# Performance work log

Measured on AMD Instinct MI355X. Metric: run time of the kernel, lower is better.

## Reference

```python
import jax, jax.numpy as jnp
import numpy as np
import math
from jax import lax

L, E, H, F = 4, 1024, 16, 4096
B, S = 8, 512
VV, VR = 40, 30
DIST_V = 200
PAD_ID = 0


def setup_inputs() -> dict:
    key = jax.random.key(0)
    ks = iter(jax.random.split(key, 32))
    w = lambda *sh: jax.random.normal(next(ks), sh, jnp.float32) * 0.02
    inp = {
        'val_emb': w(VV, E),
        'ring_emb': w(VR, E),
        'dist_emb': w(DIST_V, H),
        'Wqkv': w(L, 3 * E, E), 'bqkv': jnp.zeros((L, 3 * E), jnp.float32),
        'Wo': w(L, E, E), 'bo': jnp.zeros((L, E), jnp.float32),
        'ln1_s': jnp.ones((L, E), jnp.float32), 'ln1_b': jnp.zeros((L, E), jnp.float32),
        'W1': w(L, F, E), 'b1': jnp.zeros((L, F), jnp.float32),
        'W2': w(L, E, F), 'b2': jnp.zeros((L, E), jnp.float32),
        'ln2_s': jnp.ones((L, E), jnp.float32), 'ln2_b': jnp.zeros((L, E), jnp.float32),
        'lnf_s': jnp.ones((E,), jnp.float32), 'lnf_b': jnp.zeros((E,), jnp.float32),
        'gen_W': w(VV * VR, E), 'gen_b': jnp.zeros((VV * VR,), jnp.float32),
    }
    val = jax.random.randint(next(ks), (B, S), 0, VV)
    val = val.at[:, 0].set(1)  # ensure first key is never <pad> (id 0)
    inp['val_sequences'] = val
    inp['ring_sequences'] = jax.random.randint(next(ks), (B, S), 0, VR)
    inp['distance_squares'] = jax.random.randint(next(ks), (B, S, S), 0, DIST_V)
    return inp


def _ln(x, s, b):
    m = x.mean(-1, keepdims=True)
    v = ((x - m) ** 2).mean(-1, keepdims=True)
    return (x - m) / jnp.sqrt(v + 1e-5) * s + b


def _forward(val_emb, ring_emb, dist_emb, Wqkv, bqkv, Wo, bo, ln1_s, ln1_b,
             W1, b1, W2, b2, ln2_s, ln2_b, lnf_s, lnf_b, gen_W, gen_b,
             val_sequences, ring_sequences, distance_squares):
    Bv, Sv = val_sequences.shape
    dh = E // H
    scale = 1.0 / math.sqrt(dh)
    # token embeddings, each scaled by sqrt(emb_size)
    x = (val_emb[val_sequences] + ring_emb[ring_sequences]) * math.sqrt(E)  # [B,S,E]
    # distance bias [B,S,S,H] -> [B,H,S,S], causal fill with -inf, key padding -inf
    bias = jnp.transpose(dist_emb[distance_squares], (0, 3, 1, 2))
    causal = jnp.tril(jnp.ones((Sv, Sv), bool))
    mask = jnp.where(causal[None, None], bias, -jnp.inf)
    pad = (val_sequences == PAD_ID)  # [B,S]
    mask = jnp.where(pad[:, None, None, :], -jnp.inf, mask)

    def step(h, p):
        wqkv, bq, wo, bo_, l1s, l1b, w1, b1_, w2, b2_, l2s, l2b = p
        qkv = h @ wqkv.T + bq  # [B,S,3E]
        q, k, v = jnp.split(qkv, 3, axis=-1)
        q = q.reshape(Bv, Sv, H, dh).transpose(0, 2, 1, 3)
        k = k.reshape(Bv, Sv, H, dh).transpose(0, 2, 1, 3)
        v = v.reshape(Bv, Sv, H, dh).transpose(0, 2, 1, 3)
        scores = jnp.einsum('bhqd,bhkd->bhqk', q, k) * scale + mask
        a = jax.nn.softmax(scores, axis=-1)
        ctx = jnp.einsum('bhqk,bhkd->bhqd', a, v)
        ctx = ctx.transpose(0, 2, 1, 3).reshape(Bv, Sv, E)
        h = _ln(h + ctx @ wo.T + bo_, l1s, l1b)  # post-norm
        ff = jax.nn.gelu(h @ w1.T + b1_, approximate=False) @ w2.T + b2_
        h = _ln(h + ff, l2s, l2b)
        return h, None

    layer_params = (Wqkv, bqkv, Wo, bo, ln1_s, ln1_b, W1, b1, W2, b2, ln2_s, ln2_b)
    x, _ = lax.scan(step, x, layer_params)
    x = _ln(x, lnf_s, lnf_b)
    return x @ gen_W.T + gen_b  # [B,S,VV*VR]


def reference(val_emb, ring_emb, dist_emb, Wqkv, bqkv, Wo, bo, ln1_s, ln1_b,
              W1, b1, W2, b2, ln2_s, ln2_b, lnf_s, lnf_b, gen_W, gen_b,
              val_sequences, ring_sequences, distance_squares):
    return _forward(val_emb, ring_emb, dist_emb, Wqkv, bqkv, Wo, bo, ln1_s, ln1_b,
                    W1, b1, W2, b2, ln2_s, ln2_b, lnf_s, lnf_b, gen_W, gen_b,
                    val_sequences, ring_sequences, distance_squares)
```

## Files before the change

### kernel.cpp

```cpp
#include <hip/hip_runtime.h>
#include <hip/hip_bf16.h>

typedef __attribute__((ext_vector_type(8))) short bf16x8;
typedef __attribute__((ext_vector_type(4))) float f32x4;
typedef unsigned short u16;
typedef __attribute__((ext_vector_type(4))) unsigned short u16x4;

#define L_ 4
#define E_ 1024
#define H_ 16
#define F_ 4096
#define B_ 8
#define S_ 512
#define T_ 4096
#define GEN_N 1200
#define GEN_PAD 1280

#define AS1 __attribute__((address_space(1)))
#define AS3 __attribute__((address_space(3)))

static __device__ __forceinline__ u16 f2bf(float f) {
  unsigned u = __float_as_uint(f);
  unsigned r = (u + 0x7fffu + ((u >> 16) & 1u)) >> 16;
  return (u16)r;
}

static __device__ __forceinline__ unsigned cvt_pk_bf16(float lo, float hi) {
  unsigned r;
  asm("v_cvt_pk_bf16_f32 %0, %1, %2" : "=v"(r) : "v"(lo), "v"(hi));
  return r;
}

static __device__ __forceinline__ float fast_gelu(float v) {
  float y = 0.7978845608f * (v + 0.044715f * v * v * v);
  y = fminf(fmaxf(y, -9.f), 9.f);
  float e2 = __expf(2.f * y);
  float th = (e2 - 1.f) / (e2 + 1.f);
  return 0.5f * v * (1.f + th);
}

__global__ __launch_bounds__(256) void cvt_bf16(const float* __restrict__ src,
                                                u16* __restrict__ dst, int n) {
  int i = (blockIdx.x * 256 + threadIdx.x) * 4;
  if (i >= n) return;
  float4 v = *reinterpret_cast<const float4*>(src + i);
  u16x4 o = {f2bf(v.x), f2bf(v.y), f2bf(v.z), f2bf(v.w)};
  *reinterpret_cast<u16x4*>(dst + i) = o;
}

__global__ __launch_bounds__(256) void cvt4_k(const float* __restrict__ s0,
                                              const float* __restrict__ s1,
                                              const float* __restrict__ s2,
                                              const float* __restrict__ s3,
                                              u16* __restrict__ d0, u16* __restrict__ d1,
                                              u16* __restrict__ d2, u16* __restrict__ d3) {
  int q = blockIdx.x * 256 + threadIdx.x;
  const float* s;
  u16* d;
  int i;
  if (q < 786432) { s = s0; d = d0; i = q; }
  else if (q < 786432 + 262144) { s = s1; d = d1; i = q - 786432; }
  else if (q < 786432 + 262144 + 1048576) { s = s2; d = d2; i = q - (786432 + 262144); }
  else { s = s3; d = d3; i = q - (786432 + 262144 + 1048576); }
  i *= 4;
  float4 v = *reinterpret_cast<const float4*>(s + i);
  u16x4 o = {f2bf(v.x), f2bf(v.y), f2bf(v.z), f2bf(v.w)};
  *reinterpret_cast<u16x4*>(d + i) = o;
}

__global__ __launch_bounds__(256) void embed_k(const float* __restrict__ val_emb,
                                               const float* __restrict__ ring_emb,
                                               const int* __restrict__ vseq,
                                               const int* __restrict__ rseq,
                                               float* __restrict__ h, u16* __restrict__ xbf) {
  int tok = blockIdx.x;
  int e = threadIdx.x * 4;
  int v = vseq[tok], r = rseq[tok];
  float4 a = *reinterpret_cast<const float4*>(val_emb + v * E_ + e);
  float4 b = *reinterpret_cast<const float4*>(ring_emb + r * E_ + e);
  float4 o;
  o.x = (a.x + b.x) * 32.f; o.y = (a.y + b.y) * 32.f;
  o.z = (a.z + b.z) * 32.f; o.w = (a.w + b.w) * 32.f;
  *reinterpret_cast<float4*>(h + (size_t)tok * E_ + e) = o;
  u16x4 ob = {f2bf(o.x), f2bf(o.y), f2bf(o.z), f2bf(o.w)};
  *reinterpret_cast<u16x4*>(xbf + (size_t)tok * E_ + e) = ob;
}

__global__ __launch_bounds__(256) void ln_k(const float* hin, const float* add0,
                                            const float* add1, const float* cbias,
                                            const float* g, const float* bta,
                                            float* hout, u16* xout) {
  int tok = blockIdx.x * 4 + (threadIdx.x >> 6);
  int lane = threadIdx.x & 63;
  const float* hp = hin + (size_t)tok * E_;
  float4 v[4];
  #pragma unroll
  for (int p = 0; p < 4; ++p) {
    int e = p * 256 + lane * 4;
    v[p] = *reinterpret_cast<const float4*>(hp + e);
    if (add0) {
      float4 a0 = *reinterpret_cast<const float4*>(add0 + (size_t)tok * E_ + e);
      float4 a1 = *reinterpret_cast<const float4*>(add1 + (size_t)tok * E_ + e);
      float4 cb = *reinterpret_cast<const float4*>(cbias + e);
      v[p].x += a0.x + a1.x + cb.x; v[p].y += a0.y + a1.y + cb.y;
      v[p].z += a0.z + a1.z + cb.z; v[p].w += a0.w + a1.w + cb.w;
    }
  }
  float s = 0.f, q = 0.f;
  #pragma unroll
  for (int p = 0; p < 4; ++p) {
    s += v[p].x + v[p].y + v[p].z + v[p].w;
    q += v[p].x * v[p].x + v[p].y * v[p].y + v[p].z * v[p].z + v[p].w * v[p].w;
  }
  #pragma unroll
  for (int off = 1; off < 64; off <<= 1) {
    s += __shfl_xor(s, off, 64);
    q += __shfl_xor(q, off, 64);
  }
  float mean = s * (1.f / E_);
  float var = q * (1.f / E_) - mean * mean;
  float inv = rsqrtf(var + 1e-5f);
  #pragma unroll
  for (int p = 0; p < 4; ++p) {
    int e = p * 256 + lane * 4;
    float4 gg = *reinterpret_cast<const float4*>(g + e);
    float4 bb = *reinterpret_cast<const float4*>(bta + e);
    float4 o;
    o.x = (v[p].x - mean) * inv * gg.x + bb.x;
    o.y = (v[p].y - mean) * inv * gg.y + bb.y;
    o.z = (v[p].z - mean) * inv * gg.z + bb.z;
    o.w = (v[p].w - mean) * inv * gg.w + bb.w;
    if (hout) *reinterpret_cast<float4*>(hout + (size_t)tok * E_ + e) = o;
    u16x4 ob = {f2bf(o.x), f2bf(o.y), f2bf(o.z), f2bf(o.w)};
    *reinterpret_cast<u16x4*>(xout + (size_t)tok * E_ + e) = ob;
  }
}

template <int EPI>
__global__ __launch_bounds__(256, 2) void gemm_small(const u16* __restrict__ A,
                                                     const u16* __restrict__ W,
                                                     const float* __restrict__ bias,
                                                     void* __restrict__ Cp,
                                                     u16* __restrict__ Vt,
                                                     int M, int N, int K, int tilesN) {
  __shared__ __align__(16) char lds[49152];
  int tid = threadIdx.x;
  int wid = tid >> 6, l = tid & 63;
  int wm = wid >> 1, wn = wid & 1;
  int lr = l & 15, lk = l >> 4;
  int nwg = gridDim.x, bid = blockIdx.x;
  int swz = ((nwg & 7) == 0) ? ((bid & 7) * (nwg >> 3) + (bid >> 3)) : bid;
  int tm = swz / tilesN, tn = swz % tilesN;
  int row0 = tm * 128, col0 = tn * 256;

  int srow = tid >> 2;
  int sch = ((tid & 3) ^ ((srow >> 1) & 3)) * 8;
  const u16* gA = A + (size_t)(row0 + srow) * K + sch;
  const u16* gB = W + (size_t)(col0 + srow) * K + sch;
  int wslot = wid * 1024;

  auto stage = [&](int buf, int kt) {
    size_t ko = (size_t)kt * 32;
    int base = buf * 24576;
    #pragma unroll
    for (int i = 0; i < 2; ++i)
      __builtin_amdgcn_global_load_lds((const AS1 void*)(gA + (size_t)i * 64 * K + ko),
                                       (AS3 void*)(lds + base + i * 4096 + wslot), 16, 0, 0);
    #pragma unroll
    for (int i = 0; i < 4; ++i)
      __builtin_amdgcn_global_load_lds((const AS1 void*)(gB + (size_t)i * 64 * K + ko),
                                       (AS3 void*)(lds + base + 8192 + i * 4096 + wslot), 16, 0, 0);
  };

  int ck = (lk ^ ((lr >> 1) & 3)) * 16;
  f32x4 acc[4][8];
  f32x4 z = {0.f, 0.f, 0.f, 0.f};
  #pragma unroll
  for (int m = 0; m < 4; ++m)
    #pragma unroll
    for (int n = 0; n < 8; ++n) acc[m][n] = z;

  auto compute = [&](int buf) {
    int base = buf * 24576;
    bf16x8 bfr[8];
    #pragma unroll
    for (int n = 0; n < 8; ++n)
      bfr[n] = *reinterpret_cast<const bf16x8*>(lds + base + 8192 + (wn * 128 + n * 16 + lr) * 64 + ck);
    #pragma unroll
    for (int m = 0; m < 4; ++m) {
      bf16x8 af = *reinterpret_cast<const bf16x8*>(lds + base + (wm * 64 + m * 16 + lr) * 64 + ck);
      #pragma unroll
      for (int n = 0; n < 8; ++n)
        acc[m][n] = __builtin_amdgcn_mfma_f32_16x16x32_bf16(af, bfr[n], acc[m][n], 0, 0, 0);
    }
  };

  int nt = K >> 5;
  stage(0, 0);
  int cur = 0;
  for (int t = 0; t < nt; ++t) {
    if (t + 1 < nt) {
      stage(cur ^ 1, t + 1);
      asm volatile("s_waitcnt vmcnt(6)" ::: "memory");
    } else {
      asm volatile("s_waitcnt vmcnt(0)" ::: "memory");
    }
    __builtin_amdgcn_s_barrier();
    asm volatile("" ::: "memory");
    compute(cur);
    asm volatile("" ::: "memory");
    __builtin_amdgcn_s_barrier();
    cur ^= 1;
  }

  #pragma unroll
  for (int n = 0; n < 8; ++n) {
    int col = col0 + wn * 128 + n * 16 + lr;
    float bv = bias[col];
    #pragma unroll
    for (int m = 0; m < 4; ++m) {
      int rbase = row0 + wm * 64 + m * 16 + lk * 4;
      #pragma unroll
      for (int r2 = 0; r2 < 4; ++r2) {
        float v = acc[m][n][r2] + bv;
        if (EPI == 1) v = fast_gelu(v);
        int row = rbase + r2;
        u16 bw = f2bf(v);
        ((u16*)Cp)[(size_t)row * N + col] = bw;
        if (EPI == 0 && Vt != nullptr && col >= 2 * E_) {
          int dg = col - 2 * E_;
          int hh = dg >> 6, dd = dg & 63;
          int bb = row >> 9, ss = row & 511;
          Vt[((size_t)((bb * 16 + hh) * 64 + dd) << 9) + ss] = bw;
        }
      }
    }
  }
}

template <int EPI, int NW, int SPLITK>
__global__ __launch_bounds__(512, 2) void gemm_big(const u16* __restrict__ A,
                                                   const u16* __restrict__ W,
                                                   const float* __restrict__ bias,
                                                   void* __restrict__ Cp,
                                                   int M, int N, int K, int tilesN) {
  constexpr int BN = 64 * NW;
  __shared__ __align__(16) u16 As[2][256 * 64];
  __shared__ __align__(16) u16 Bs[2][BN * 64];
  int tid = threadIdx.x;
  int wid = tid >> 6, ln = tid & 63;
  int wm = wid >> 2, wn = wid & 3;
  int lr = ln & 15, lk = ln >> 4;
  int nwg = gridDim.x;
  int bid = blockIdx.x;
  int swz = ((nwg & 7) == 0) ? ((bid & 7) * (nwg >> 3) + (bid >> 3)) : bid;
  int sp = 0, tile = swz;
  if (SPLITK > 1) { sp = swz & (SPLITK - 1); tile = swz / SPLITK; }
  int tm = tile / tilesN, tn = tile % tilesN;
  int row0 = tm * 256, col0 = tn * BN;
  int Ks = K / SPLITK;
  int kbase = sp * Ks;

  int srow = tid >> 3;
  int schunk = ((tid & 7) ^ (srow & 7)) * 8;
  const u16* gA = A + (size_t)(row0 + srow) * K + kbase + schunk;
  const u16* gB = W + (size_t)(col0 + srow) * K + kbase + schunk;
  size_t ldsBase = (size_t)((wid << 3) * 64) * 2;

  auto stage = [&](int buf, int kt) {
    size_t ko = (size_t)kt * 64;
    #pragma unroll
    for (int i = 0; i < 4; ++i)
      __builtin_amdgcn_global_load_lds(
          (const AS1 void*)(gA + (size_t)i * 64 * K + ko),
          (AS3 void*)((char*)&As[buf][0] + ldsBase + (size_t)i * 64 * 128), 16, 0, 0);
    #pragma unroll
    for (int i = 0; i < NW; ++i)
      __builtin_amdgcn_global_load_lds(
          (const AS1 void*)(gB + (size_t)i * 64 * K + ko),
          (AS3 void*)((char*)&Bs[buf][0] + ldsBase + (size_t)i * 64 * 128), 16, 0, 0);
  };

  f32x4 acc[8][NW];
  f32x4 z = {0.f, 0.f, 0.f, 0.f};
  #pragma unroll
  for (int m = 0; m < 8; ++m)
    #pragma unroll
    for (int n = 0; n < NW; ++n) acc[m][n] = z;

  auto compute = [&](int buf) {
    #pragma unroll
    for (int s = 0; s < 2; ++s) {
      int ch = ((s * 4 + lk) ^ (lr & 7)) * 8;
      bf16x8 bfr[NW];
      #pragma unroll
      for (int n = 0; n < NW; ++n)
        bfr[n] = *reinterpret_cast<const bf16x8*>(&Bs[buf][(wn * (16 * NW) + n * 16 + lr) * 64 + ch]);
      #pragma unroll
      for (int m = 0; m < 8; ++m) {
        bf16x8 af = *reinterpret_cast<const bf16x8*>(&As[buf][(wm * 128 + m * 16 + lr) * 64 + ch]);
        #pragma unroll
        for (int n = 0; n < NW; ++n)
          acc[m][n] = __builtin_amdgcn_mfma_f32_16x16x32_bf16(af, bfr[n], acc[m][n], 0, 0, 0);
      }
    }
  };

  int nt = Ks >> 6;
  stage(0, 0);
  int cur = 0;
  for (int t = 0; t < nt; ++t) {
    if (t + 1 < nt) {
      stage(cur ^ 1, t + 1);
      if constexpr (NW == 2) asm volatile("s_waitcnt vmcnt(6)" ::: "memory");
      else if constexpr (NW == 3) asm volatile("s_waitcnt vmcnt(7)" ::: "memory");
      else asm volatile("s_waitcnt vmcnt(8)" ::: "memory");
    } else {
      asm volatile("s_waitcnt vmcnt(0)" ::: "memory");
    }
    __builtin_amdgcn_s_barrier();
    asm volatile("" ::: "memory");
    compute(cur);
    asm volatile("" ::: "memory");
    __builtin_amdgcn_s_barrier();
    cur ^= 1;
  }

  #pragma unroll
  for (int n = 0; n < NW; ++n) {
    int col = col0 + wn * (16 * NW) + n * 16 + lr;
    if (col >= N) continue;
    float bv = (EPI == 2) ? 0.f : bias[col];
    #pragma unroll
    for (int m = 0; m < 8; ++m) {
      int rbase = row0 + wm * 128 + m * 16 + lk * 4;
      #pragma unroll
      for (int r2 = 0; r2 < 4; ++r2) {
        float v = acc[m][n][r2] + bv;
        int row = rbase + r2;
        if (EPI == 2)
          ((float*)Cp)[(size_t)sp * M * N + (size_t)row * N + col] = v;
        else
          ((float*)Cp)[(size_t)row * N + col] = v;
      }
    }
  }
}

__global__ __launch_bounds__(256, 4) void attn_fused_k(const u16* __restrict__ qkv,
                                                       const int* __restrict__ dist,
                                                       const float* __restrict__ dist_emb,
                                                       const int* __restrict__ vseq,
                                                       const u16* __restrict__ Vt,
                                                       u16* __restrict__ ctx) {
  int blk = blockIdx.x;
  int bh = blk & 127;
  int qt = blk >> 7;
  int b = bh >> 4, h = bh & 15;
  int tid = threadIdx.x, wv = tid >> 6, l = tid & 63;
  int lr = l & 15, lk = l >> 4;

  __shared__ float de[208];
  __shared__ unsigned char padf[512];
  __shared__ unsigned char d8[64 * 516];

  int ncol = (qt + 1) * 64;
  for (int i = tid; i < 208; i += 256)
    de[i] = (i < 200) ? dist_emb[i * H_ + h] : -1e30f;
  for (int i = tid; i < (ncol >> 2); i += 256) {
    int4 v = *reinterpret_cast<const int4*>(vseq + b * S_ + i * 4);
    uchar4 pz;
    pz.x = (v.x == 0); pz.y = (v.y == 0); pz.z = (v.z == 0); pz.w = (v.w == 0);
    *reinterpret_cast<uchar4*>(&padf[i * 4]) = pz;
  }
  __syncthreads();

  {
    int r = tid >> 2;
    const int* drow = dist + ((size_t)(b * S_ + qt * 64 + r) << 9);
    int nc4 = ncol >> 2;
    for (int c4 = (tid & 3); c4 < nc4; c4 += 4) {
      int4 dv = *reinterpret_cast<const int4*>(drow + c4 * 4);
      uchar4 o;
      o.x = padf[c4 * 4 + 0] ? (unsigned char)200 : (unsigned char)dv.x;
      o.y = padf[c4 * 4 + 1] ? (unsigned char)200 : (unsigned char)dv.y;
      o.z = padf[c4 * 4 + 2] ? (unsigned char)200 : (unsigned char)dv.z;
      o.w = padf[c4 * 4 + 3] ? (unsigned char)200 : (unsigned char)dv.w;
      *reinterpret_cast<uchar4*>(&d8[r * 516 + c4 * 4]) = o;
    }
  }
  __syncthreads();

  int q0 = qt * 64 + wv * 16;
  int nv = 4 * qt + wv + 1;
  int qglob = q0 + lr;
  int qloc = wv * 16 + lr;

  bf16x8 aq0 = *reinterpret_cast<const bf16x8*>(
      qkv + (size_t)(b * S_ + q0 + lr) * 3072 + h * 64 + lk * 8);
  bf16x8 aq1 = *reinterpret_cast<const bf16x8*>(
      qkv + (size_t)(b * S_ + q0 + lr) * 3072 + h * 64 + 32 + lk * 8);

  float sm = 0.f;
  f32x4 z = {0.f, 0.f, 0.f, 0.f};
  f32x4 acc_o[4] = {z, z, z, z};

  int sA = lr + ((2 * lk) & 3) * 16;
  int sB = lr + ((2 * lk + 1) & 3) * 16;
  int jsel = (lk >= 2);

  int ngroups = (nv + 1) >> 1;
  #pragma unroll 1
  for (int g = 0; g < ngroups; ++g) {
    f32x4 s0 = z, s1 = z;
    {
      int n = 2 * g;
      const u16* kb = qkv + (size_t)(b * S_ + n * 16 + lr) * 3072 + E_ + h * 64 + lk * 8;
      bf16x8 bk0 = *reinterpret_cast<const bf16x8*>(kb);
      bf16x8 bk1 = *reinterpret_cast<const bf16x8*>(kb + 32);
      s0 = __builtin_amdgcn_mfma_f32_16x16x32_bf16(bk0, aq0, s0, 0, 0, 0);
      s0 = __builtin_amdgcn_mfma_f32_16x16x32_bf16(bk1, aq1, s0, 0, 0, 0);
    }
    if (2 * g + 1 < nv) {
      int n = 2 * g + 1;
      const u16* kb = qkv + (size_t)(b * S_ + n * 16 + lr) * 3072 + E_ + h * 64 + lk * 8;
      bf16x8 bk0 = *reinterpret_cast<const bf16x8*>(kb);
      bf16x8 bk1 = *reinterpret_cast<const bf16x8*>(kb + 32);
      s1 = __builtin_amdgcn_mfma_f32_16x16x32_bf16(bk0, aq0, s1, 0, 0, 0);
      s1 = __builtin_amdgcn_mfma_f32_16x16x32_bf16(bk1, aq1, s1, 0, 0, 0);
    }
    float e0[4], e1[4];
    #pragma unroll
    for (int r2 = 0; r2 < 4; ++r2) {
      int kg0 = (2 * g) * 16 + lk * 4 + r2;
      float e = 0.f;
      if (kg0 <= qglob) {
        int d = d8[qloc * 516 + kg0];
        e = __expf(s0[r2] * 0.125f + de[d]);
      }
      e0[r2] = e; sm += e;
    }
    #pragma unroll
    for (int r2 = 0; r2 < 4; ++r2) {
      int kg1 = (2 * g + 1) * 16 + lk * 4 + r2;
      float e = 0.f;
      if (2 * g + 1 < nv && kg1 <= qglob) {
        int d = d8[qloc * 516 + kg1];
        e = __expf(s1[r2] * 0.125f + de[d]);
      }
      e1[r2] = e; sm += e;
    }
    unsigned t0p0 = cvt_pk_bf16(e0[0], e0[1]);
    unsigned t0p1 = cvt_pk_bf16(e0[2], e0[3]);
    unsigned t1p0 = cvt_pk_bf16(e1[0], e1[1]);
    unsigned t1p1 = cvt_pk_bf16(e1[2], e1[3]);
    unsigned a00 = __shfl((int)t0p0, sA, 64), a10 = __shfl((int)t1p0, sA, 64);
    unsigned a01 = __shfl((int)t0p1, sA, 64), a11 = __shfl((int)t1p1, sA, 64);
    unsigned b00 = __shfl((int)t0p0, sB, 64), b10 = __shfl((int)t1p0, sB, 64);
    unsigned b01 = __shfl((int)t0p1, sB, 64), b11 = __shfl((int)t1p1, sB, 64);
    unsigned w0 = jsel ? a10 : a00;
    unsigned w1 = jsel ? a11 : a01;
    unsigned w2 = jsel ? b10 : b00;
    unsigned w3 = jsel ? b11 : b01;
    bf16x8 pfrag;
    {
      unsigned pw[4] = {w0, w1, w2, w3};
      pfrag = *reinterpret_cast<bf16x8*>(pw);
    }
    #pragma unroll
    for (int n4 = 0; n4 < 4; ++n4) {
      bf16x8 vf = *reinterpret_cast<const bf16x8*>(
          Vt + (size_t)(bh * 64 + n4 * 16 + lr) * S_ + g * 32 + lk * 8);
      acc_o[n4] = __builtin_amdgcn_mfma_f32_16x16x32_bf16(vf, pfrag, acc_o[n4], 0, 0, 0);
    }
  }

  sm += __shfl_xor(sm, 16, 64);
  sm += __shfl_xor(sm, 32, 64);
  float il = 1.f / sm;

  #pragma unroll
  for (int n4 = 0; n4 < 4; ++n4) {
    u16x4 o;
    o.x = f2bf(acc_o[n4][0] * il);
    o.y = f2bf(acc_o[n4][1] * il);
    o.z = f2bf(acc_o[n4][2] * il);
    o.w = f2bf(acc_o[n4][3] * il);
    *reinterpret_cast<u16x4*>(ctx + (size_t)(b * S_ + qglob) * E_ + h * 64 + n4 * 16 + lk * 4) = o;
  }
}

extern "C" void kernel_launch(void* const* d_in, const int* in_sizes, int n_in,
                              void* d_out, int out_size, void* d_ws, size_t ws_size,
                              hipStream_t stream) {
  const float* val_emb = (const float*)d_in[0];
  const float* ring_emb = (const float*)d_in[1];
  const float* dist_emb = (const float*)d_in[2];
  const float* Wqkv = (const float*)d_in[3];
  const float* bqkv = (const float*)d_in[4];
  const float* Wo = (const float*)d_in[5];
  const float* bo = (const float*)d_in[6];
  const float* ln1_s = (const float*)d_in[7];
  const float* ln1_b = (const float*)d_in[8];
  const float* W1 = (const float*)d_in[9];
  const float* b1 = (const float*)d_in[10];
  const float* W2 = (const float*)d_in[11];
  const float* b2 = (const float*)d_in[12];
  const float* ln2_s = (const float*)d_in[13];
  const float* ln2_b = (const float*)d_in[14];
  const float* lnf_s = (const float*)d_in[15];
  const float* lnf_b = (const float*)d_in[16];
  const float* gen_W = (const float*)d_in[17];
  const float* gen_b = (const float*)d_in[18];
  const int* vseq = (const int*)d_in[19];
  const int* rseq = (const int*)d_in[20];
  const int* dist = (const int*)d_in[21];

  char* ws = (char*)d_ws;
  size_t off = 0;
  auto alloc = [&](size_t nbytes) {
    char* p = ws + off;
    off += (nbytes + 255) & ~(size_t)255;
    return p;
  };
  u16* gw_bf = (u16*)alloc((size_t)GEN_PAD * E_ * 2);
  u16* wqkv_l = (u16*)alloc((size_t)3 * E_ * E_ * 2);
  u16* wo_l = (u16*)alloc((size_t)E_ * E_ * 2);
  u16* w1_l = (u16*)alloc((size_t)F_ * E_ * 2);
  u16* w2_l = (u16*)alloc((size_t)E_ * F_ * 2);
  float* h = (float*)alloc((size_t)T_ * E_ * 4);
  u16* x_bf = (u16*)alloc((size_t)T_ * E_ * 2);
  u16* qkv_bf = (u16*)alloc((size_t)T_ * 3 * E_ * 2);
  u16* ctx_bf = (u16*)alloc((size_t)T_ * E_ * 2);
  u16* vt_bf = (u16*)alloc((size_t)B_ * H_ * 64 * S_ * 2);
  u16* p_bf = (u16*)alloc((size_t)B_ * H_ * S_ * S_ * 2);
  u16* ff_bf = p_bf;
  float* psum = (float*)(p_bf + (size_t)T_ * F_);
  (void)ws_size; (void)in_sizes; (void)n_in; (void)out_size; (void)rseq;

  cvt_bf16<<<dim3((GEN_N * E_ / 4 + 255) / 256), dim3(256), 0, stream>>>(gen_W, gw_bf,
                                                                         GEN_N * E_);
  embed_k<<<dim3(T_), dim3(256), 0, stream>>>(val_emb, ring_emb, vseq, rseq, h, x_bf);

  for (int l = 0; l < L_; ++l) {
    cvt4_k<<<dim3(12288), dim3(256), 0, stream>>>(
        Wqkv + (size_t)l * 3 * E_ * E_, Wo + (size_t)l * E_ * E_,
        W1 + (size_t)l * F_ * E_, W2 + (size_t)l * E_ * F_,
        wqkv_l, wo_l, w1_l, w2_l);

    gemm_small<0><<<dim3(384), dim3(256), 0, stream>>>(
        x_bf, wqkv_l, bqkv + (size_t)l * 3 * E_, qkv_bf, vt_bf, T_, 3 * E_, E_, 12);
    attn_fused_k<<<dim3(B_ * H_ * 8), dim3(256), 0, stream>>>(qkv_bf, dist, dist_emb,
                                                              vseq, vt_bf, ctx_bf);
    gemm_big<2, 2, 2><<<dim3(256), dim3(512), 0, stream>>>(
        ctx_bf, wo_l, nullptr, psum, T_, E_, E_, 8);
    ln_k<<<dim3(T_ / 4), dim3(256), 0, stream>>>(h, psum, psum + (size_t)T_ * E_,
                                                 bo + (size_t)l * E_,
                                                 ln1_s + (size_t)l * E_, ln1_b + (size_t)l * E_,
                                                 h, x_bf);
    gemm_small<1><<<dim3(512), dim3(256), 0, stream>>>(
        x_bf, w1_l, b1 + (size_t)l * F_, ff_bf, nullptr, T_, F_, E_, 16);
    gemm_big<2, 2, 2><<<dim3(256), dim3(512), 0, stream>>>(
        ff_bf, w2_l, nullptr, psum, T_, E_, F_, 8);
    ln_k<<<dim3(T_ / 4), dim3(256), 0, stream>>>(h, psum, psum + (size_t)T_ * E_,
                                                 b2 + (size_t)l * E_,
                                                 ln2_s + (size_t)l * E_, ln2_b + (size_t)l * E_,
                                                 h, x_bf);
  }
  ln_k<<<dim3(T_ / 4), dim3(256), 0, stream>>>(h, nullptr, nullptr, nullptr, lnf_s, lnf_b,
                                               nullptr, x_bf);
  gemm_big<3, 2, 1><<<dim3(160), dim3(512), 0, stream>>>(
      x_bf, gw_bf, gen_b, (float*)d_out, T_, GEN_N, E_, 10);
}
```

Baseline: 1.047 ms.

## Precompute padded uint8 distance table once and read it directly in attention

Adds a one-time kernel that converts int32 distance indices into a uint8 table, with padded keys mapped to a sentinel. This is shared across all layers and heads. The attention kernel then loads these bytes straight from global memory instead of rebuilding an LDS copy per block. Dropping the large LDS buffer allows launch bounds to request 8 blocks per CU. The cost is a 2 MB workspace buffer and uncoalesced 4-byte global loads inside the inner loop.

```diff
diff --git a/kernel.cpp b/kernel.cpp
--- a/kernel.cpp
+++ b/kernel.cpp
@@ -66,6 +66,22 @@
   float4 v = *reinterpret_cast<const float4*>(s + i);
   u16x4 o = {f2bf(v.x), f2bf(v.y), f2bf(v.z), f2bf(v.w)};
   *reinterpret_cast<u16x4*>(d + i) = o;
+}
+
+__global__ __launch_bounds__(256) void d8pre_k(const int* __restrict__ dist,
+                                               const int* __restrict__ vseq,
+                                               unsigned char* __restrict__ d8g) {
+  int idx = blockIdx.x * 256 + threadIdx.x;
+  int k4 = idx & 127;
+  int b = idx >> 16;
+  int4 dv = *reinterpret_cast<const int4*>(dist + (size_t)idx * 4);
+  int4 vv = *reinterpret_cast<const int4*>(vseq + b * S_ + k4 * 4);
+  uchar4 o;
+  o.x = (vv.x == 0) ? (unsigned char)200 : (unsigned char)dv.x;
+  o.y = (vv.y == 0) ? (unsigned char)200 : (unsigned char)dv.y;
+  o.z = (vv.z == 0) ? (unsigned char)200 : (unsigned char)dv.z;
+  o.w = (vv.w == 0) ? (unsigned char)200 : (unsigned char)dv.w;
+  *reinterpret_cast<uchar4*>(d8g + (size_t)idx * 4) = o;
 }
 
 __global__ __launch_bounds__(256) void embed_k(const float* __restrict__ val_emb,
@@ -347,10 +363,9 @@
   }
 }
 
-__global__ __launch_bounds__(256, 4) void attn_fused_k(const u16* __restrict__ qkv,
-                                                       const int* __restrict__ dist,
+__global__ __launch_bounds__(256, 8) void attn_fused_k(const u16* __restrict__ qkv,
+                                                       const unsigned char* __restrict__ d8g,
                                                        const float* __restrict__ dist_emb,
-                                                       const int* __restrict__ vseq,
                                                        const u16* __restrict__ Vt,
                                                        u16* __restrict__ ctx) {
   int blk = blockIdx.x;
@@ -361,40 +376,14 @@
   int lr = l & 15, lk = l >> 4;
 
   __shared__ float de[208];
-  __shared__ unsigned char padf[512];
-  __shared__ unsigned char d8[64 * 516];
-
-  int ncol = (qt + 1) * 64;
   for (int i = tid; i < 208; i += 256)
     de[i] = (i < 200) ? dist_emb[i * H_ + h] : -1e30f;
-  for (int i = tid; i < (ncol >> 2); i += 256) {
-    int4 v = *reinterpret_cast<const int4*>(vseq + b * S_ + i * 4);
-    uchar4 pz;
-    pz.x = (v.x == 0); pz.y = (v.y == 0); pz.z = (v.z == 0); pz.w = (v.w == 0);
-    *reinterpret_cast<uchar4*>(&padf[i * 4]) = pz;
-  }
-  __syncthreads();
-
-  {
-    int r = tid >> 2;
-    const int* drow = dist + ((size_t)(b * S_ + qt * 64 + r) << 9);
-    int nc4 = ncol >> 2;
-    for (int c4 = (tid & 3); c4 < nc4; c4 += 4) {
-      int4 dv = *reinterpret_cast<const int4*>(drow + c4 * 4);
-      uchar4 o;
-      o.x = padf[c4 * 4 + 0] ? (unsigned char)200 : (unsigned char)dv.x;
-      o.y = padf[c4 * 4 + 1] ? (unsigned char)200 : (unsigned char)dv.y;
-      o.z = padf[c4 * 4 + 2] ? (unsigned char)200 : (unsigned char)dv.z;
-      o.w = padf[c4 * 4 + 3] ? (unsigned char)200 : (unsigned char)dv.w;
-      *reinterpret_cast<uchar4*>(&d8[r * 516 + c4 * 4]) = o;
-    }
-  }
   __syncthreads();
 
   int q0 = qt * 64 + wv * 16;
   int nv = 4 * qt + wv + 1;
   int qglob = q0 + lr;
-  int qloc = wv * 16 + lr;
+  const unsigned char* drow = d8g + ((size_t)(b * S_ + qglob) << 9);
 
   bf16x8 aq0 = *reinterpret_cast<const bf16x8*>(
       qkv + (size_t)(b * S_ + q0 + lr) * 3072 + h * 64 + lk * 8);
@@ -408,47 +397,50 @@
   int sA = lr + ((2 * lk) & 3) * 16;
   int sB = lr + ((2 * lk + 1) & 3) * 16;
   int jsel = (lk >= 2);
+
+  const u16* kBase = qkv + (size_t)(b * S_ + lr) * 3072 + E_ + h * 64 + lk * 8;
+  const u16* vBase = Vt + (size_t)(bh * 64 + lr) * S_ + lk * 8;
 
   int ngroups = (nv + 1) >> 1;
   #pragma unroll 1
   for (int g = 0; g < ngroups; ++g) {
     f32x4 s0 = z, s1 = z;
     {
-      int n = 2 * g;
-      const u16* kb = qkv + (size_t)(b * S_ + n * 16 + lr) * 3072 + E_ + h * 64 + lk * 8;
+      const u16* kb = kBase + (size_t)(2 * g) * 16 * 3072;
       bf16x8 bk0 = *reinterpret_cast<const bf16x8*>(kb);
       bf16x8 bk1 = *reinterpret_cast<const bf16x8*>(kb + 32);
       s0 = __builtin_amdgcn_mfma_f32_16x16x32_bf16(bk0, aq0, s0, 0, 0, 0);
       s0 = __builtin_amdgcn_mfma_f32_16x16x32_bf16(bk1, aq1, s0, 0, 0, 0);
     }
     if (2 * g + 1 < nv) {
-      int n = 2 * g + 1;
-      const u16* kb = qkv + (size_t)(b * S_ + n * 16 + lr) * 3072 + E_ + h * 64 + lk * 8;
+      const u16* kb = kBase + (size_t)(2 * g + 1) * 16 * 3072;
       bf16x8 bk0 = *reinterpret_cast<const bf16x8*>(kb);
       bf16x8 bk1 = *reinterpret_cast<const bf16x8*>(kb + 32);
       s1 = __builtin_amdgcn_mfma_f32_16x16x32_bf16(bk0, aq0, s1, 0, 0, 0);
       s1 = __builtin_amdgcn_mfma_f32_16x16x32_bf16(bk1, aq1, s1, 0, 0, 0);
     }
     float e0[4], e1[4];
-    #pragma unroll
-    for (int r2 = 0; r2 < 4; ++r2) {
-      int kg0 = (2 * g) * 16 + lk * 4 + r2;
-      float e = 0.f;
-      if (kg0 <= qglob) {
-        int d = d8[qloc * 516 + kg0];
-        e = __expf(s0[r2] * 0.125f + de[d]);
+    {
+      unsigned dd = *reinterpret_cast<const unsigned*>(drow + (2 * g) * 16 + lk * 4);
+      #pragma unroll
+      for (int r2 = 0; r2 < 4; ++r2) {
+        int kg = (2 * g) * 16 + lk * 4 + r2;
+        float e = 0.f;
+        if (kg <= qglob)
+          e = __expf(s0[r2] * 0.125f + de[(dd >> (8 * r2)) & 255]);
+        e0[r2] = e; sm += e;
       }
-      e0[r2] = e; sm += e;
-    }
-    #pragma unroll
-    for (int r2 = 0; r2 < 4; ++r2) {
-      int kg1 = (2 * g + 1) * 16 + lk * 4 + r2;
-      float e = 0.f;
-      if (2 * g + 1 < nv && kg1 <= qglob) {
-        int d = d8[qloc * 516 + kg1];
-        e = __expf(s1[r2] * 0.125f + de[d]);
+    }
+    {
+      unsigned dd = *reinterpret_cast<const unsigned*>(drow + (2 * g + 1) * 16 + lk * 4);
+      #pragma unroll
+      for (int r2 = 0; r2 < 4; ++r2) {
+        int kg = (2 * g + 1) * 16 + lk * 4 + r2;
+        float e = 0.f;
+        if (2 * g + 1 < nv && kg <= qglob)
+          e = __expf(s1[r2] * 0.125f + de[(dd >> (8 * r2)) & 255]);
+        e1[r2] = e; sm += e;
       }
-      e1[r2] = e; sm += e;
     }
     unsigned t0p0 = cvt_pk_bf16(e0[0], e0[1]);
     unsigned t0p1 = cvt_pk_bf16(e0[2], e0[3]);
@@ -467,12 +459,15 @@
       unsigned pw[4] = {w0, w1, w2, w3};
       pfrag = *reinterpret_cast<bf16x8*>(pw);
     }
-    #pragma unroll
-    for (int n4 = 0; n4 < 4; ++n4) {
-      bf16x8 vf = *reinterpret_cast<const bf16x8*>(
-          Vt + (size_t)(bh * 64 + n4 * 16 + lr) * S_ + g * 32 + lk * 8);
-      acc_o[n4] = __builtin_amdgcn_mfma_f32_16x16x32_bf16(vf, pfrag, acc_o[n4], 0, 0, 0);
-    }
+    const u16* vb = vBase + g * 32;
+    acc_o[0] = __builtin_amdgcn_mfma_f32_16x16x32_bf16(
+        *reinterpret_cast<const bf16x8*>(vb), pfrag, acc_o[0], 0, 0, 0);
+    acc_o[1] = __builtin_amdgcn_mfma_f32_16x16x32_bf16(
+        *reinterpret_cast<const bf16x8*>(vb + 16 * S_), pfrag, acc_o[1], 0, 0, 0);
+    acc_o[2] = __builtin_amdgcn_mfma_f32_16x16x32_bf16(
+        *reinterpret_cast<const bf16x8*>(vb + 32 * S_), pfrag, acc_o[2], 0, 0, 0);
+    acc_o[3] = __builtin_amdgcn_mfma_f32_16x16x32_bf16(
+        *reinterpret_cast<const bf16x8*>(vb + 48 * S_), pfrag, acc_o[3], 0, 0, 0);
   }
 
   sm += __shfl_xor(sm, 16, 64);
@@ -533,6 +528,7 @@
   u16* qkv_bf = (u16*)alloc((size_t)T_ * 3 * E_ * 2);
   u16* ctx_bf = (u16*)alloc((size_t)T_ * E_ * 2);
   u16* vt_bf = (u16*)alloc((size_t)B_ * H_ * 64 * S_ * 2);
+  unsigned char* d8g = (unsigned char*)alloc((size_t)B_ * S_ * S_);
   u16* p_bf = (u16*)alloc((size_t)B_ * H_ * S_ * S_ * 2);
   u16* ff_bf = p_bf;
   float* psum = (float*)(p_bf + (size_t)T_ * F_);
@@ -540,6 +536,7 @@
 
   cvt_bf16<<<dim3((GEN_N * E_ / 4 + 255) / 256), dim3(256), 0, stream>>>(gen_W, gw_bf,
                                                                          GEN_N * E_);
+  d8pre_k<<<dim3(B_ * S_ * S_ / 4 / 256), dim3(256), 0, stream>>>(dist, vseq, d8g);
   embed_k<<<dim3(T_), dim3(256), 0, stream>>>(val_emb, ring_emb, vseq, rseq, h, x_bf);
 
   for (int l = 0; l < L_; ++l) {
@@ -550,8 +547,8 @@
 
     gemm_small<0><<<dim3(384), dim3(256), 0, stream>>>(
         x_bf, wqkv_l, bqkv + (size_t)l * 3 * E_, qkv_bf, vt_bf, T_, 3 * E_, E_, 12);
-    attn_fused_k<<<dim3(B_ * H_ * 8), dim3(256), 0, stream>>>(qkv_bf, dist, dist_emb,
-                                                              vseq, vt_bf, ctx_bf);
+    attn_fused_k<<<dim3(B_ * H_ * 8), dim3(256), 0, stream>>>(qkv_bf, d8g, dist_emb,
+                                                              vt_bf, ctx_bf);
     gemm_big<2, 2, 2><<<dim3(256), dim3(512), 0, stream>>>(
         ctx_bf, wo_l, nullptr, psum, T_, E_, E_, 8);
     ln_k<<<dim3(T_ / 4), dim3(256), 0, stream>>>(h, psum, psum + (size_t)T_ * E_,
```

Measured after the change: 1.061 ms. No clear change (+1.3%).
